# Kernel tuning notes

Measured on AMD Instinct MI355X. Metric: run time of the kernel, lower is better.

## Reference

```python
import jax, jax.numpy as jnp
import numpy as np

TOP_K = 2
AUX_COEFF = 0.01

def setup_inputs() -> dict:
    key = jax.random.key(0)
    k1, k2, k3, k4 = jax.random.split(key, 4)
    B, T, d, E = 4, 1024, 1024, 8
    x = jax.random.normal(k1, (B, T, d), dtype=jnp.float32)
    w_gate = jax.random.normal(k2, (d, E), dtype=jnp.float32) * 0.02
    w1 = jax.random.normal(k3, (E, d, 4 * d), dtype=jnp.float32) * 0.02
    w2 = jax.random.normal(k4, (E, 4 * d, d), dtype=jnp.float32) * 0.02
    return {"x": x, "w_gate": w_gate, "w1": w1, "w2": w2}

def reference(x, w_gate, w1, w2):
    B, T, d = x.shape
    E = w_gate.shape[1]
    N = B * T
    xf = x.reshape(N, d)

    # Router: softmax over experts, top-k, renormalize
    logits = xf @ w_gate                      # [N, E]
    probs = jax.nn.softmax(logits, axis=-1)   # [N, E]
    topk_p, topk_i = jax.lax.top_k(probs, TOP_K)
    topk_p = topk_p / topk_p.sum(axis=-1, keepdims=True)

    # Combine weights: scatter top-k probs into [N, E] (equiv. to masked scatter-add loop)
    comb = jnp.zeros((N, E), dtype=x.dtype).at[
        jnp.arange(N)[:, None], topk_i].add(topk_p)

    # Grouped expert MLP (dense over experts, weighted combine)
    h = jnp.einsum('nd,edf->enf', xf, w1)     # [E, N, 4d]
    h = jax.nn.gelu(h, approximate=False)     # exact erf GELU like nn.GELU
    y = jnp.einsum('enf,efd->end', h, w2)     # [E, N, d]
    out = jnp.einsum('ne,end->nd', comb, y).reshape(B, T, d)

    # Load-balancing aux loss (training branch)
    counts = jnp.zeros((E,), dtype=x.dtype).at[topk_i.reshape(-1)].add(1.0)
    f = counts / (N * TOP_K)
    p = probs.mean(axis=0)
    aux_loss = AUX_COEFF * E * jnp.sum(f * p)
    return out, aux_loss
```

## Files before the change

kernel.cpp:

```cpp
#include <hip/hip_runtime.h>
#include <cmath>

#define N_TOK 4096
#define DDIM 1024
#define FDIM 4096
#define NEXP 8
#define MAXT 72
#define MAXROWS (MAXT * 128)

typedef __attribute__((ext_vector_type(4))) float f32x4;
typedef __attribute__((ext_vector_type(8))) __bf16 bf16x8;
typedef __attribute__((ext_vector_type(4))) unsigned short us4;
typedef __attribute__((ext_vector_type(8))) unsigned short us8;

__device__ __forceinline__ unsigned short f2bf(float f) {
  unsigned u = __builtin_bit_cast(unsigned, f);
  u += 0x7FFFu + ((u >> 16) & 1u);
  return (unsigned short)(u >> 16);
}

__device__ __forceinline__ void gload16(const void* g, void* l) {
  __builtin_amdgcn_global_load_lds(
      (const __attribute__((address_space(1))) unsigned int*)g,
      (__attribute__((address_space(3))) unsigned int*)l, 16, 0, 0);
}

__global__ __launch_bounds__(64) void router_kernel(
    const float* __restrict__ x, const float* __restrict__ wg,
    float* __restrict__ probs, int* __restrict__ eids, float* __restrict__ ewts) {
  int n = blockIdx.x;
  int t = threadIdx.x;
  const float* xr = x + (size_t)n * DDIM;
  float acc[8] = {0, 0, 0, 0, 0, 0, 0, 0};
  for (int k = t; k < DDIM; k += 64) {
    float xv = xr[k];
    const float* wr = wg + k * 8;
#pragma unroll
    for (int e = 0; e < 8; e++) acc[e] = fmaf(xv, wr[e], acc[e]);
  }
#pragma unroll
  for (int off = 32; off > 0; off >>= 1) {
#pragma unroll
    for (int e = 0; e < 8; e++) acc[e] += __shfl_xor(acc[e], off, 64);
  }
  if (t == 0) {
    float mx = acc[0];
#pragma unroll
    for (int e = 1; e < 8; e++) mx = fmaxf(mx, acc[e]);
    float p[8], s = 0.f;
#pragma unroll
    for (int e = 0; e < 8; e++) { p[e] = expf(acc[e] - mx); s += p[e]; }
    float inv = 1.f / s;
#pragma unroll
    for (int e = 0; e < 8; e++) { p[e] *= inv; probs[n * 8 + e] = p[e]; }
    int i0 = 0;
#pragma unroll
    for (int e = 1; e < 8; e++) if (p[e] > p[i0]) i0 = e;
    int i1 = (i0 == 0) ? 1 : 0;
#pragma unroll
    for (int e = 0; e < 8; e++) if (e != i0 && p[e] > p[i1]) i1 = e;
    float sw = p[i0] + p[i1];
    eids[n * 2] = i0; eids[n * 2 + 1] = i1;
    ewts[n * 2] = p[i0] / sw; ewts[n * 2 + 1] = p[i1] / sw;
  }
}

__global__ __launch_bounds__(256) void plan_kernel(
    const float* __restrict__ probs, const int* __restrict__ eids,
    float* __restrict__ aux_out, int* __restrict__ meta) {
  __shared__ float pl[256][8];
  __shared__ int cl[256][8];
  __shared__ float ps2[8];
  __shared__ int cn2[8];
  int t = threadIdx.x;
  float pa[8] = {0, 0, 0, 0, 0, 0, 0, 0};
  int ca[8] = {0, 0, 0, 0, 0, 0, 0, 0};
  for (int n = t; n < N_TOK; n += 256) {
#pragma unroll
    for (int e = 0; e < 8; e++) pa[e] += probs[n * 8 + e];
    ca[eids[n * 2]]++; ca[eids[n * 2 + 1]]++;
  }
#pragma unroll
  for (int e = 0; e < 8; e++) { pl[t][e] = pa[e]; cl[t][e] = ca[e]; }
  __syncthreads();
  if (t < 8) {
    float s = 0; int c = 0;
    for (int i = 0; i < 256; i++) { s += pl[i][t]; c += cl[i][t]; }
    ps2[t] = s; cn2[t] = c;
  }
  __syncthreads();
  if (t == 0) {
    int tb = 0; float aux = 0.f;
    for (int e = 0; e < 8; e++) {
      int c = cn2[e];
      meta[e] = c; meta[8 + e] = 0; meta[16 + e] = tb;
      int tiles = (c + 127) >> 7;
      for (int i = 0; i < tiles; i++) meta[24 + tb + i] = e;
      tb += tiles;
      aux += ((float)c / (float)(N_TOK * 2)) * (ps2[e] / (float)N_TOK);
    }
    meta[96] = tb;
    *aux_out = 0.01f * 8.f * aux;
  }
}

__global__ __launch_bounds__(256) void scatter_kernel(
    const int* __restrict__ eids, int* __restrict__ meta,
    int* __restrict__ perm, int* __restrict__ inv) {
  int n = blockIdx.x * 256 + threadIdx.x;
  if (n >= N_TOK) return;
#pragma unroll
  for (int s = 0; s < 2; s++) {
    int e = eids[n * 2 + s];
    int pos = atomicAdd(&meta[8 + e], 1);
    int row = (meta[16 + e] << 7) + pos;
    perm[row] = n;
    inv[n * 2 + s] = row;
  }
}

__global__ __launch_bounds__(256) void convert_x_kernel(
    const float* __restrict__ x, unsigned short* __restrict__ xb) {
  int i = blockIdx.x * 256 + threadIdx.x;
  f32x4 v = ((const f32x4*)x)[i];
  us4 o = {f2bf(v[0]), f2bf(v[1]), f2bf(v[2]), f2bf(v[3])};
  ((us4*)xb)[i] = o;
}

__global__ __launch_bounds__(256) void transpose_conv(
    const float* __restrict__ src, unsigned short* __restrict__ dst, int R, int C) {
  __shared__ unsigned short tile[64 * 64];
  size_t eoff = (size_t)blockIdx.z * (size_t)R * (size_t)C;
  src += eoff; dst += eoff;
  int c0 = blockIdx.x << 6, r0 = blockIdx.y << 6;
  int t = threadIdx.x;
  int rl = (t >> 4) << 2;
  int cl = (t & 15) << 2;
  f32x4 v[4];
#pragma unroll
  for (int i = 0; i < 4; i++)
    v[i] = *(const f32x4*)(src + (size_t)(r0 + rl + i) * C + c0 + cl);
#pragma unroll
  for (int u = 0; u < 4; u++) {
    int c = cl + u;
    us4 o = {f2bf(v[0][u]), f2bf(v[1][u]), f2bf(v[2][u]), f2bf(v[3][u])};
    unsigned byteoff = (unsigned)c * 128 + ((((unsigned)(rl >> 3)) ^ (unsigned)(c & 7)) << 4) + (unsigned)(rl & 7) * 2;
    *(us4*)((char*)tile + byteoff) = o;
  }
  __syncthreads();
#pragma unroll
  for (int p = 0; p < 2; p++) {
    int id = t + p * 256;
    int c = id >> 3, q = id & 7;
    unsigned byteoff = (unsigned)c * 128 + (((unsigned)q ^ (unsigned)(c & 7)) << 4);
    us8 val = *(const us8*)((const char*)tile + byteoff);
    *(us8*)(dst + (size_t)(c0 + c) * R + r0 + q * 8) = val;
  }
}

__global__ __launch_bounds__(256, 2) void gemm1_kernel(
    const unsigned short* __restrict__ A,
    const unsigned short* __restrict__ Bt,
    unsigned short* __restrict__ Hout,
    const int* __restrict__ perm,
    const int* __restrict__ tileExpert, const int* __restrict__ totalTiles) {
  constexpr int K = DDIM, NB = FDIM;
  __shared__ unsigned short ldsA[128 * 64];
  __shared__ unsigned short ldsB[256 * 64];
  int tile = blockIdx.x;
  if (tile >= *totalTiles) return;
  int e = tileExpert[tile];
  int m0 = tile << 7;
  int n0 = blockIdx.y << 8;
  const unsigned short* Bbase = Bt + ((size_t)e * NB + n0) * K;
  int t = threadIdx.x;
  int wave = t >> 6, lane = t & 63;
  int g = lane >> 4, ln = lane & 15;
  int wm = wave >> 1, wn = wave & 1;

  const unsigned short* srcA[4];
  const unsigned short* srcB[8];
  unsigned loffA[4], loffB[8];
#pragma unroll
  for (int i = 0; i < 4; i++) {
    int c = wave * 256 + i * 64 + lane;
    int r = c >> 3, kc = c & 7;
    srcA[i] = A + (size_t)perm[m0 + r] * K + ((kc ^ (r & 7)) << 3);
    loffA[i] = (unsigned)(wave * 256 + i * 64) * 16u;
  }
#pragma unroll
  for (int i = 0; i < 8; i++) {
    int c = wave * 512 + i * 64 + lane;
    int r = c >> 3, kc = c & 7;
    srcB[i] = Bbase + (size_t)r * K + ((kc ^ (r & 7)) << 3);
    loffB[i] = (unsigned)(wave * 512 + i * 64) * 16u;
  }

  f32x4 acc[4][8];
#pragma unroll
  for (int a = 0; a < 4; a++)
#pragma unroll
    for (int b = 0; b < 8; b++) acc[a][b] = (f32x4){0.f, 0.f, 0.f, 0.f};

  for (int k0 = 0; k0 < K; k0 += 64) {
#pragma unroll
    for (int i = 0; i < 4; i++) gload16(srcA[i] + k0, (char*)ldsA + loffA[i]);
#pragma unroll
    for (int i = 0; i < 8; i++) gload16(srcB[i] + k0, (char*)ldsB + loffB[i]);
    __syncthreads();
#pragma unroll
    for (int ks = 0; ks < 2; ks++) {
      bf16x8 af[4], bfr[8];
      int q = ks * 4 + g;
#pragma unroll
      for (int mf = 0; mf < 4; mf++) {
        int m = wm * 64 + mf * 16 + ln;
        af[mf] = *(const bf16x8*)((const char*)ldsA + m * 128 + ((q ^ (m & 7)) << 4));
      }
#pragma unroll
      for (int nf = 0; nf < 8; nf++) {
        int n = wn * 128 + nf * 16 + ln;
        bfr[nf] = *(const bf16x8*)((const char*)ldsB + n * 128 + ((q ^ (n & 7)) << 4));
      }
#pragma unroll
      for (int mf = 0; mf < 4; mf++)
#pragma unroll
        for (int nf = 0; nf < 8; nf++)
          acc[mf][nf] = __builtin_amdgcn_mfma_f32_16x16x32_bf16(af[mf], bfr[nf], acc[mf][nf], 0, 0, 0);
    }
    __syncthreads();
  }

#pragma unroll
  for (int mf = 0; mf < 4; mf++) {
#pragma unroll
    for (int r = 0; r < 4; r++) {
      int row = m0 + wm * 64 + mf * 16 + g * 4 + r;
      unsigned short* hp = Hout + (size_t)row * NB + n0 + wn * 128 + ln;
#pragma unroll
      for (int nf = 0; nf < 8; nf++) {
        float v = acc[mf][nf][r];
        v = 0.5f * v * (1.f + erff(v * 0.70710678118654752f));
        hp[nf * 16] = f2bf(v);
      }
    }
  }
}

__global__ __launch_bounds__(256, 2) void gemm2_kernel(
    const unsigned short* __restrict__ A,
    const unsigned short* __restrict__ Bt,
    float* __restrict__ Out,
    const int* __restrict__ tileExpert, const int* __restrict__ totalTiles) {
  constexpr int K = FDIM, NB = DDIM;
  __shared__ unsigned short ldsA[128 * 64];
  __shared__ unsigned short ldsB[128 * 64];
  int tile = blockIdx.x;
  if (tile >= *totalTiles) return;
  int e = tileExpert[tile];
  int m0 = tile << 7;
  int n0 = blockIdx.y << 7;
  const unsigned short* Bbase = Bt + ((size_t)e * NB + n0) * K;
  int t = threadIdx.x;
  int wave = t >> 6, lane = t & 63;
  int g = lane >> 4, ln = lane & 15;
  int wm = wave >> 1, wn = wave & 1;

  const unsigned short* srcA[4];
  const unsigned short* srcB[4];
#pragma unroll
  for (int i = 0; i < 4; i++) {
    int c = wave * 256 + i * 64 + lane;
    int r = c >> 3, kc = c & 7;
    srcA[i] = A + (size_t)(m0 + r) * K + ((kc ^ (r & 7)) << 3);
    srcB[i] = Bbase + (size_t)r * K + ((kc ^ (r & 7)) << 3);
  }

  f32x4 acc[4][4];
#pragma unroll
  for (int a = 0; a < 4; a++)
#pragma unroll
    for (int b = 0; b < 4; b++) acc[a][b] = (f32x4){0.f, 0.f, 0.f, 0.f};

  for (int k0 = 0; k0 < K; k0 += 64) {
#pragma unroll
    for (int i = 0; i < 4; i++) {
      int cb = wave * 256 + i * 64;
      gload16(srcA[i] + k0, &ldsA[cb * 8]);
      gload16(srcB[i] + k0, &ldsB[cb * 8]);
    }
    __syncthreads();
#pragma unroll
    for (int ks = 0; ks < 2; ks++) {
      bf16x8 af[4], bfr[4];
      int q = ks * 4 + g;
#pragma unroll
      for (int mf = 0; mf < 4; mf++) {
        int m = wm * 64 + mf * 16 + ln;
        af[mf] = *(const bf16x8*)((const char*)ldsA + m * 128 + ((q ^ (m & 7)) << 4));
      }
#pragma unroll
      for (int nf = 0; nf < 4; nf++) {
        int n = wn * 64 + nf * 16 + ln;
        bfr[nf] = *(const bf16x8*)((const char*)ldsB + n * 128 + ((q ^ (n & 7)) << 4));
      }
#pragma unroll
      for (int mf = 0; mf < 4; mf++)
#pragma unroll
        for (int nf = 0; nf < 4; nf++)
          acc[mf][nf] = __builtin_amdgcn_mfma_f32_16x16x32_bf16(af[mf], bfr[nf], acc[mf][nf], 0, 0, 0);
    }
    __syncthreads();
  }

#pragma unroll
  for (int mf = 0; mf < 4; mf++) {
#pragma unroll
    for (int r = 0; r < 4; r++) {
      int row = m0 + wm * 64 + mf * 16 + g * 4 + r;
      float* yp = Out + (size_t)row * NB + n0 + wn * 64 + ln;
#pragma unroll
      for (int nf = 0; nf < 4; nf++) yp[nf * 16] = acc[mf][nf][r];
    }
  }
}

__global__ __launch_bounds__(256) void combine_kernel(
    const float* __restrict__ yscr, const int* __restrict__ inv,
    const float* __restrict__ ewts, float* __restrict__ out) {
  int n = blockIdx.x, t = threadIdx.x;
  int r0 = inv[n * 2], r1 = inv[n * 2 + 1];
  float w0 = ewts[n * 2], w1 = ewts[n * 2 + 1];
  f32x4 a = *(const f32x4*)(yscr + (size_t)r0 * DDIM + t * 4);
  f32x4 b = *(const f32x4*)(yscr + (size_t)r1 * DDIM + t * 4);
  f32x4 o;
#pragma unroll
  for (int j = 0; j < 4; j++) o[j] = w0 * a[j] + w1 * b[j];
  *(f32x4*)(out + (size_t)n * DDIM + t * 4) = o;
}

extern "C" void kernel_launch(void* const* d_in, const int* in_sizes, int n_in,
                              void* d_out, int out_size, void* d_ws, size_t ws_size,
                              hipStream_t stream) {
  const float* x = (const float*)d_in[0];
  const float* wgate = (const float*)d_in[1];
  const float* w1 = (const float*)d_in[2];
  const float* w2 = (const float*)d_in[3];
  float* out = (float*)d_out;

  char* w = (char*)d_ws;
  float* probs = (float*)w;                 w += (size_t)N_TOK * 8 * 4;
  int* eids = (int*)w;                      w += (size_t)N_TOK * 2 * 4;
  float* ewts = (float*)w;                  w += (size_t)N_TOK * 2 * 4;
  int* meta = (int*)w;                      w += 512;
  int* perm = (int*)w;                      w += (size_t)MAXROWS * 4;
  int* inv = (int*)w;                       w += (size_t)N_TOK * 2 * 4;
  unsigned short* xb = (unsigned short*)w;  w += (size_t)N_TOK * DDIM * 2;
  unsigned short* w1t = (unsigned short*)w; w += (size_t)NEXP * DDIM * FDIM * 2;
  unsigned short* w2t = (unsigned short*)w; w += (size_t)NEXP * DDIM * FDIM * 2;
  unsigned short* h = (unsigned short*)w;   w += (size_t)MAXROWS * FDIM * 2;
  float* yscr = (float*)w1t;

  hipMemsetAsync(perm, 0, (size_t)MAXROWS * 4, stream);

  router_kernel<<<N_TOK, 64, 0, stream>>>(x, wgate, probs, eids, ewts);
  plan_kernel<<<1, 256, 0, stream>>>(probs, eids, out + 4194304, meta);
  scatter_kernel<<<16, 256, 0, stream>>>(eids, meta, perm, inv);
  convert_x_kernel<<<4096, 256, 0, stream>>>(x, xb);
  transpose_conv<<<dim3(64, 16, 8), 256, 0, stream>>>(w1, w1t, DDIM, FDIM);
  transpose_conv<<<dim3(16, 64, 8), 256, 0, stream>>>(w2, w2t, FDIM, DDIM);
  gemm1_kernel<<<dim3(MAXT, 16), 256, 0, stream>>>(
      xb, w1t, h, perm, meta + 24, meta + 96);
  gemm2_kernel<<<dim3(MAXT, 8), 256, 0, stream>>>(
      h, w2t, yscr, meta + 24, meta + 96);
  combine_kernel<<<N_TOK, 256, 0, stream>>>(yscr, inv, ewts, out);
}
```

Measured before the change: 424.9 us.

## Fuse x bf16 conversion into router, shrink gemm1 tile, split-K gemm2

```diff
diff --git a/kernel.cpp b/kernel.cpp
--- a/kernel.cpp
+++ b/kernel.cpp
@@ -27,16 +27,30 @@
 
 __global__ __launch_bounds__(64) void router_kernel(
     const float* __restrict__ x, const float* __restrict__ wg,
-    float* __restrict__ probs, int* __restrict__ eids, float* __restrict__ ewts) {
+    float* __restrict__ probs, int* __restrict__ eids, float* __restrict__ ewts,
+    unsigned short* __restrict__ xb) {
   int n = blockIdx.x;
   int t = threadIdx.x;
   const float* xr = x + (size_t)n * DDIM;
+  f32x4 xv[4];
+#pragma unroll
+  for (int j = 0; j < 4; j++) xv[j] = *(const f32x4*)(xr + j * 256 + t * 4);
   float acc[8] = {0, 0, 0, 0, 0, 0, 0, 0};
-  for (int k = t; k < DDIM; k += 64) {
-    float xv = xr[k];
-    const float* wr = wg + k * 8;
-#pragma unroll
-    for (int e = 0; e < 8; e++) acc[e] = fmaf(xv, wr[e], acc[e]);
+#pragma unroll
+  for (int j = 0; j < 4; j++) {
+#pragma unroll
+    for (int u = 0; u < 4; u++) {
+      float v = xv[j][u];
+      const float* wr = wg + (size_t)(j * 256 + t * 4 + u) * 8;
+#pragma unroll
+      for (int e = 0; e < 8; e++) acc[e] = fmaf(v, wr[e], acc[e]);
+    }
+  }
+  unsigned short* xo = xb + (size_t)n * DDIM;
+#pragma unroll
+  for (int j = 0; j < 4; j++) {
+    us4 o = {f2bf(xv[j][0]), f2bf(xv[j][1]), f2bf(xv[j][2]), f2bf(xv[j][3])};
+    *(us4*)(xo + j * 256 + t * 4) = o;
   }
 #pragma unroll
   for (int off = 32; off > 0; off >>= 1) {
@@ -119,14 +133,6 @@
   }
 }
 
-__global__ __launch_bounds__(256) void convert_x_kernel(
-    const float* __restrict__ x, unsigned short* __restrict__ xb) {
-  int i = blockIdx.x * 256 + threadIdx.x;
-  f32x4 v = ((const f32x4*)x)[i];
-  us4 o = {f2bf(v[0]), f2bf(v[1]), f2bf(v[2]), f2bf(v[3])};
-  ((us4*)xb)[i] = o;
-}
-
 __global__ __launch_bounds__(256) void transpose_conv(
     const float* __restrict__ src, unsigned short* __restrict__ dst, int R, int C) {
   __shared__ unsigned short tile[64 * 64];
@@ -166,12 +172,12 @@
     const int* __restrict__ tileExpert, const int* __restrict__ totalTiles) {
   constexpr int K = DDIM, NB = FDIM;
   __shared__ unsigned short ldsA[128 * 64];
-  __shared__ unsigned short ldsB[256 * 64];
+  __shared__ unsigned short ldsB[128 * 64];
   int tile = blockIdx.x;
   if (tile >= *totalTiles) return;
   int e = tileExpert[tile];
   int m0 = tile << 7;
-  int n0 = blockIdx.y << 8;
+  int n0 = blockIdx.y << 7;
   const unsigned short* Bbase = Bt + ((size_t)e * NB + n0) * K;
   int t = threadIdx.x;
   int wave = t >> 6, lane = t & 63;
@@ -179,38 +185,32 @@
   int wm = wave >> 1, wn = wave & 1;
 
   const unsigned short* srcA[4];
-  const unsigned short* srcB[8];
-  unsigned loffA[4], loffB[8];
+  const unsigned short* srcB[4];
 #pragma unroll
   for (int i = 0; i < 4; i++) {
     int c = wave * 256 + i * 64 + lane;
     int r = c >> 3, kc = c & 7;
     srcA[i] = A + (size_t)perm[m0 + r] * K + ((kc ^ (r & 7)) << 3);
-    loffA[i] = (unsigned)(wave * 256 + i * 64) * 16u;
-  }
-#pragma unroll
-  for (int i = 0; i < 8; i++) {
-    int c = wave * 512 + i * 64 + lane;
-    int r = c >> 3, kc = c & 7;
     srcB[i] = Bbase + (size_t)r * K + ((kc ^ (r & 7)) << 3);
-    loffB[i] = (unsigned)(wave * 512 + i * 64) * 16u;
-  }
-
-  f32x4 acc[4][8];
+  }
+
+  f32x4 acc[4][4];
 #pragma unroll
   for (int a = 0; a < 4; a++)
 #pragma unroll
-    for (int b = 0; b < 8; b++) acc[a][b] = (f32x4){0.f, 0.f, 0.f, 0.f};
+    for (int b = 0; b < 4; b++) acc[a][b] = (f32x4){0.f, 0.f, 0.f, 0.f};
 
   for (int k0 = 0; k0 < K; k0 += 64) {
 #pragma unroll
-    for (int i = 0; i < 4; i++) gload16(srcA[i] + k0, (char*)ldsA + loffA[i]);
-#pragma unroll
-    for (int i = 0; i < 8; i++) gload16(srcB[i] + k0, (char*)ldsB + loffB[i]);
+    for (int i = 0; i < 4; i++) {
+      int cb = wave * 256 + i * 64;
+      gload16(srcA[i] + k0, &ldsA[cb * 8]);
+      gload16(srcB[i] + k0, &ldsB[cb * 8]);
+    }
     __syncthreads();
 #pragma unroll
     for (int ks = 0; ks < 2; ks++) {
-      bf16x8 af[4], bfr[8];
+      bf16x8 af[4], bfr[4];
       int q = ks * 4 + g;
 #pragma unroll
       for (int mf = 0; mf < 4; mf++) {
@@ -218,14 +218,14 @@
         af[mf] = *(const bf16x8*)((const char*)ldsA + m * 128 + ((q ^ (m & 7)) << 4));
       }
 #pragma unroll
-      for (int nf = 0; nf < 8; nf++) {
-        int n = wn * 128 + nf * 16 + ln;
+      for (int nf = 0; nf < 4; nf++) {
+        int n = wn * 64 + nf * 16 + ln;
         bfr[nf] = *(const bf16x8*)((const char*)ldsB + n * 128 + ((q ^ (n & 7)) << 4));
       }
 #pragma unroll
       for (int mf = 0; mf < 4; mf++)
 #pragma unroll
-        for (int nf = 0; nf < 8; nf++)
+        for (int nf = 0; nf < 4; nf++)
           acc[mf][nf] = __builtin_amdgcn_mfma_f32_16x16x32_bf16(af[mf], bfr[nf], acc[mf][nf], 0, 0, 0);
     }
     __syncthreads();
@@ -236,9 +236,9 @@
 #pragma unroll
     for (int r = 0; r < 4; r++) {
       int row = m0 + wm * 64 + mf * 16 + g * 4 + r;
-      unsigned short* hp = Hout + (size_t)row * NB + n0 + wn * 128 + ln;
-#pragma unroll
-      for (int nf = 0; nf < 8; nf++) {
+      unsigned short* hp = Hout + (size_t)row * NB + n0 + wn * 64 + ln;
+#pragma unroll
+      for (int nf = 0; nf < 4; nf++) {
         float v = acc[mf][nf][r];
         v = 0.5f * v * (1.f + erff(v * 0.70710678118654752f));
         hp[nf * 16] = f2bf(v);
@@ -247,12 +247,13 @@
   }
 }
 
+template <int NSLICE>
 __global__ __launch_bounds__(256, 2) void gemm2_kernel(
     const unsigned short* __restrict__ A,
     const unsigned short* __restrict__ Bt,
-    float* __restrict__ Out,
+    float* __restrict__ P0, float* __restrict__ P1,
     const int* __restrict__ tileExpert, const int* __restrict__ totalTiles) {
-  constexpr int K = FDIM, NB = DDIM;
+  constexpr int K = FDIM, NB = DDIM, KB = K / NSLICE;
   __shared__ unsigned short ldsA[128 * 64];
   __shared__ unsigned short ldsB[128 * 64];
   int tile = blockIdx.x;
@@ -260,7 +261,10 @@
   int e = tileExpert[tile];
   int m0 = tile << 7;
   int n0 = blockIdx.y << 7;
-  const unsigned short* Bbase = Bt + ((size_t)e * NB + n0) * K;
+  int z = blockIdx.z;
+  int kbase = z * KB;
+  float* Out = z ? P1 : P0;
+  const unsigned short* Bbase = Bt + ((size_t)e * NB + n0) * K + kbase;
   int t = threadIdx.x;
   int wave = t >> 6, lane = t & 63;
   int g = lane >> 4, ln = lane & 15;
@@ -272,7 +276,7 @@
   for (int i = 0; i < 4; i++) {
     int c = wave * 256 + i * 64 + lane;
     int r = c >> 3, kc = c & 7;
-    srcA[i] = A + (size_t)(m0 + r) * K + ((kc ^ (r & 7)) << 3);
+    srcA[i] = A + (size_t)(m0 + r) * K + kbase + ((kc ^ (r & 7)) << 3);
     srcB[i] = Bbase + (size_t)r * K + ((kc ^ (r & 7)) << 3);
   }
 
@@ -282,7 +286,7 @@
 #pragma unroll
     for (int b = 0; b < 4; b++) acc[a][b] = (f32x4){0.f, 0.f, 0.f, 0.f};
 
-  for (int k0 = 0; k0 < K; k0 += 64) {
+  for (int k0 = 0; k0 < KB; k0 += 64) {
 #pragma unroll
     for (int i = 0; i < 4; i++) {
       int cb = wave * 256 + i * 64;
@@ -325,14 +329,22 @@
   }
 }
 
+template <bool SPLIT>
 __global__ __launch_bounds__(256) void combine_kernel(
-    const float* __restrict__ yscr, const int* __restrict__ inv,
-    const float* __restrict__ ewts, float* __restrict__ out) {
+    const float* __restrict__ P0, const float* __restrict__ P1,
+    const int* __restrict__ inv, const float* __restrict__ ewts,
+    float* __restrict__ out) {
   int n = blockIdx.x, t = threadIdx.x;
   int r0 = inv[n * 2], r1 = inv[n * 2 + 1];
   float w0 = ewts[n * 2], w1 = ewts[n * 2 + 1];
-  f32x4 a = *(const f32x4*)(yscr + (size_t)r0 * DDIM + t * 4);
-  f32x4 b = *(const f32x4*)(yscr + (size_t)r1 * DDIM + t * 4);
+  f32x4 a = *(const f32x4*)(P0 + (size_t)r0 * DDIM + t * 4);
+  f32x4 b = *(const f32x4*)(P0 + (size_t)r1 * DDIM + t * 4);
+  if (SPLIT) {
+    f32x4 a1 = *(const f32x4*)(P1 + (size_t)r0 * DDIM + t * 4);
+    f32x4 b1 = *(const f32x4*)(P1 + (size_t)r1 * DDIM + t * 4);
+#pragma unroll
+    for (int j = 0; j < 4; j++) { a[j] += a1[j]; b[j] += b1[j]; }
+  }
   f32x4 o;
 #pragma unroll
   for (int j = 0; j < 4; j++) o[j] = w0 * a[j] + w1 * b[j];
@@ -359,19 +371,27 @@
   unsigned short* w1t = (unsigned short*)w; w += (size_t)NEXP * DDIM * FDIM * 2;
   unsigned short* w2t = (unsigned short*)w; w += (size_t)NEXP * DDIM * FDIM * 2;
   unsigned short* h = (unsigned short*)w;   w += (size_t)MAXROWS * FDIM * 2;
-  float* yscr = (float*)w1t;
+  float* yscr0 = (float*)w1t;
+  float* yscr1 = (float*)w;
+  size_t need = (size_t)(w - (char*)d_ws) + (size_t)MAXROWS * DDIM * 4;
+  bool split = ws_size >= need;
 
   hipMemsetAsync(perm, 0, (size_t)MAXROWS * 4, stream);
 
-  router_kernel<<<N_TOK, 64, 0, stream>>>(x, wgate, probs, eids, ewts);
+  router_kernel<<<N_TOK, 64, 0, stream>>>(x, wgate, probs, eids, ewts, xb);
   plan_kernel<<<1, 256, 0, stream>>>(probs, eids, out + 4194304, meta);
   scatter_kernel<<<16, 256, 0, stream>>>(eids, meta, perm, inv);
-  convert_x_kernel<<<4096, 256, 0, stream>>>(x, xb);
   transpose_conv<<<dim3(64, 16, 8), 256, 0, stream>>>(w1, w1t, DDIM, FDIM);
   transpose_conv<<<dim3(16, 64, 8), 256, 0, stream>>>(w2, w2t, FDIM, DDIM);
-  gemm1_kernel<<<dim3(MAXT, 16), 256, 0, stream>>>(
+  gemm1_kernel<<<dim3(MAXT, 32), 256, 0, stream>>>(
       xb, w1t, h, perm, meta + 24, meta + 96);
-  gemm2_kernel<<<dim3(MAXT, 8), 256, 0, stream>>>(
-      h, w2t, yscr, meta + 24, meta + 96);
-  combine_kernel<<<N_TOK, 256, 0, stream>>>(yscr, inv, ewts, out);
-}
+  if (split) {
+    gemm2_kernel<2><<<dim3(MAXT, 8, 2), 256, 0, stream>>>(
+        h, w2t, yscr0, yscr1, meta + 24, meta + 96);
+    combine_kernel<true><<<N_TOK, 256, 0, stream>>>(yscr0, yscr1, inv, ewts, out);
+  } else {
+    gemm2_kernel<1><<<dim3(MAXT, 8, 1), 256, 0, stream>>>(
+        h, w2t, yscr0, yscr0, meta + 24, meta + 96);
+    combine_kernel<false><<<N_TOK, 256, 0, stream>>>(yscr0, yscr0, inv, ewts, out);
+  }
+}
```

New measurement: 414.4 us. 1.03x faster.
